# Kernel tuning notes

Hardware: AMD Instinct MI355X
Metric: run time of the kernel (lower is better)

Reference implementation:

```python
import jax, jax.numpy as jnp
import numpy as np

D_MODEL = 1024
N_HEADS = 16
D_K = D_MODEL // N_HEADS
THETA = 10000.0
BATCH, SEQ = 4, 2048


def apply_rope(x, pos, theta=THETA):
    # x: [B, H, S, d_k]; pos: [S] int. Rotate interleaved pairs (x_{2i}, x_{2i+1}).
    half = x.shape[-1] // 2
    inv_freq = theta ** (-jnp.arange(half, dtype=x.dtype) * 2.0 / x.shape[-1])  # [half]
    ang = pos.astype(x.dtype)[:, None] * inv_freq[None, :]                      # [S, half]
    cos, sin = jnp.cos(ang), jnp.sin(ang)
    x1, x2 = x[..., 0::2], x[..., 1::2]
    r1 = x1 * cos - x2 * sin
    r2 = x1 * sin + x2 * cos
    return jnp.stack([r1, r2], axis=-1).reshape(x.shape)


def setup_inputs() -> dict:
    key = jax.random.key(0)
    k1, k2, k3 = jax.random.split(key, 3)
    x = jax.random.normal(k1, (BATCH, SEQ, D_MODEL), dtype=jnp.float32)
    W_qkv = jax.random.normal(k2, (3 * D_MODEL, D_MODEL), dtype=jnp.float32) * (D_MODEL ** -0.5)
    b_qkv = jnp.zeros((3 * D_MODEL,), dtype=jnp.float32)
    W_o = jax.random.normal(k3, (D_MODEL, D_MODEL), dtype=jnp.float32) * (D_MODEL ** -0.5)
    b_o = jnp.zeros((D_MODEL,), dtype=jnp.float32)
    token_positions = jnp.arange(SEQ, dtype=jnp.int64 if jax.config.jax_enable_x64 else jnp.int32)
    return {"x": x, "token_positions": token_positions, "W_qkv": W_qkv,
            "b_qkv": b_qkv, "W_o": W_o, "b_o": b_o}


def reference(x, token_positions, W_qkv, b_qkv, W_o, b_o):
    B, S, _ = x.shape
    qkv = x @ W_qkv.T + b_qkv                                   # [B, S, 3*d_model]
    qkv = qkv.reshape(B, S, 3, N_HEADS, D_K)
    qkv = jnp.transpose(qkv, (2, 0, 3, 1, 4))                   # [3, B, H, S, d_k]
    q, k, v = qkv[0], qkv[1], qkv[2]
    q = apply_rope(q, token_positions)
    k = apply_rope(k, token_positions)
    scores = jnp.einsum('bhqd,bhkd->bhqk', q / jnp.sqrt(jnp.asarray(D_K, x.dtype)), k)
    causal = jnp.tril(jnp.ones((S, S), dtype=bool))             # True where attended
    scores = jnp.where(causal, scores, jnp.asarray(-jnp.inf, scores.dtype))
    attn = jax.nn.softmax(scores, axis=-1)
    out = jnp.einsum('bhqk,bhkd->bhqd', attn, v)                # [B, H, S, d_k]
    out = jnp.transpose(out, (0, 2, 1, 3)).reshape(B, S, D_MODEL)
    return out @ W_o.T + b_o
```

## Files before the change

### kernel.cpp

```cpp
#include <hip/hip_runtime.h>
#include <hip/hip_bf16.h>
#include <cstdint>

#define S_LEN 2048
#define NHEAD 16
#define DMODEL 1024

using short8 = __attribute__((ext_vector_type(8))) short;
using f32x4  = __attribute__((ext_vector_type(4))) float;

__device__ __forceinline__ float bf2f(ushort u) {
    return __uint_as_float(((uint32_t)u) << 16);
}
__device__ __forceinline__ ushort f2bf(float f) {
    uint32_t u = __float_as_uint(f);
    u += 0x7FFF + ((u >> 16) & 1);
    return (ushort)(u >> 16);
}
__device__ __forceinline__ uint32_t cvt_pk_bf16(float lo, float hi) {
    uint32_t r;
    asm("v_cvt_pk_bf16_f32 %0, %1, %2" : "=v"(r) : "v"(lo), "v"(hi));
    return r;
}
__device__ __forceinline__ float exp2_(float x) {
    float r; asm("v_exp_f32 %0, %1" : "=v"(r) : "v"(x)); return r;
}

__global__ void k_cast(const float* __restrict__ in, ushort* __restrict__ out, int n4) {
    int i = blockIdx.x * blockDim.x + threadIdx.x;
    if (i < n4) {
        const float4 v = reinterpret_cast<const float4*>(in)[i];
        ushort4 o;
        o.x = f2bf(v.x); o.y = f2bf(v.y); o.z = f2bf(v.z); o.w = f2bf(v.w);
        reinterpret_cast<ushort4*>(out)[i] = o;
    }
}

__device__ __forceinline__ void gl16(const ushort* g, ushort* l) {
    __builtin_amdgcn_global_load_lds(
        (const __attribute__((address_space(1))) void*)g,
        (__attribute__((address_space(3))) void*)l, 16, 0, 0);
}

template<int OUT_BF16>
__global__ __launch_bounds__(256, 2)
void k_gemm_bt(const ushort* __restrict__ A, const ushort* __restrict__ Bm,
               const float* __restrict__ bias, void* __restrict__ Cout,
               int M, int N, int K)
{
    __shared__ ushort As[128 * 32];
    __shared__ ushort Bs[128 * 32];
    const int t = threadIdx.x;
    const int w = t >> 6, l = t & 63;
    const int lr = l & 15, lg = l >> 4;
    const int bm = blockIdx.y * 128, bn = blockIdx.x * 128;
    const int wr = (w >> 1) * 64, wc = (w & 1) * 64;

    f32x4 acc[4][4] = {};

    const ushort* ag = A + (size_t)(bm + (t >> 2)) * K + (t & 3) * 8;
    const ushort* bg = Bm + (size_t)(bn + (t >> 2)) * K + (t & 3) * 8;
    ushort* asd = &As[t * 8];
    ushort* bsd = &Bs[t * 8];
    const size_t rowskip = (size_t)64 * K;

    for (int k0 = 0; k0 < K; k0 += 32) {
        gl16(ag + k0, asd);
        gl16(ag + rowskip + k0, asd + 2048);
        gl16(bg + k0, bsd);
        gl16(bg + rowskip + k0, bsd + 2048);
        __syncthreads();
        short8 af[4], bf[4];
        #pragma unroll
        for (int m = 0; m < 4; ++m)
            af[m] = *reinterpret_cast<const short8*>(&As[(wr + m * 16 + lr) * 32 + lg * 8]);
        #pragma unroll
        for (int n = 0; n < 4; ++n)
            bf[n] = *reinterpret_cast<const short8*>(&Bs[(wc + n * 16 + lr) * 32 + lg * 8]);
        #pragma unroll
        for (int m = 0; m < 4; ++m)
            #pragma unroll
            for (int n = 0; n < 4; ++n)
                acc[m][n] = __builtin_amdgcn_mfma_f32_16x16x32_bf16(af[m], bf[n], acc[m][n], 0, 0, 0);
        __syncthreads();
    }

    const int col0 = bn + wc + lr;
    float bv[4];
    #pragma unroll
    for (int n = 0; n < 4; ++n) bv[n] = bias[col0 + n * 16];
    #pragma unroll
    for (int m = 0; m < 4; ++m) {
        const int row0 = bm + wr + m * 16 + lg * 4;
        #pragma unroll
        for (int r = 0; r < 4; ++r) {
            const size_t ro = (size_t)(row0 + r) * N;
            #pragma unroll
            for (int n = 0; n < 4; ++n) {
                float v = acc[m][n][r] + bv[n];
                if (OUT_BF16) ((ushort*)Cout)[ro + col0 + n * 16] = f2bf(v);
                else          ((float*)Cout)[ro + col0 + n * 16] = v;
            }
        }
    }
}

__global__ __launch_bounds__(256)
void k_rope_scatter(const ushort* __restrict__ qkv, const int* __restrict__ pos,
                    ushort* __restrict__ Qo, ushort* __restrict__ Ko, ushort* __restrict__ Vt)
{
    __shared__ ushort vlds[64][72];
    const int blk = blockIdx.x;
    const int st = blk & 31, bh = blk >> 5;
    const int b = bh >> 4, h = bh & 15;
    const int t = threadIdx.x;
    const int sl = t >> 2, dc = (t & 3) << 4;
    const int s = st * 64 + sl;
    const size_t base = (size_t)(b * S_LEN + s) * 3072 + h * 64 + dc;
    const float p = (float)pos[s];

    float cs[8], sn[8];
    #pragma unroll
    for (int j = 0; j < 8; ++j) {
        const int fi = (dc >> 1) + j;
        const float invf = __expf(-(float)fi * 0.28782313662425572f);
        __sincosf(p * invf, &sn[j], &cs[j]);
    }

    #pragma unroll
    for (int type = 0; type < 2; ++type) {
        union { uint4 u[2]; ushort us[16]; } in_, out_;
        in_.u[0] = *(const uint4*)(qkv + base + type * 1024);
        in_.u[1] = *(const uint4*)(qkv + base + type * 1024 + 8);
        const float scale = (type == 0) ? 0.125f * 1.44269504088896f : 1.0f;
        #pragma unroll
        for (int j = 0; j < 8; ++j) {
            float x1 = bf2f(in_.us[2 * j]), x2 = bf2f(in_.us[2 * j + 1]);
            out_.us[2 * j]     = f2bf((x1 * cs[j] - x2 * sn[j]) * scale);
            out_.us[2 * j + 1] = f2bf((x1 * sn[j] + x2 * cs[j]) * scale);
        }
        ushort* dst = (type == 0 ? Qo : Ko) + ((size_t)(bh * S_LEN + s)) * 64 + dc;
        *(uint4*)dst = out_.u[0];
        *(uint4*)(dst + 8) = out_.u[1];
    }

    {
        uint4 v0 = *(const uint4*)(qkv + base + 2048);
        uint4 v1 = *(const uint4*)(qkv + base + 2048 + 8);
        *(uint4*)&vlds[sl][dc] = v0;
        *(uint4*)&vlds[sl][dc + 8] = v1;
    }
    __syncthreads();
    {
        const int d = t >> 2, sc0 = (t & 3) << 4;
        union { uint4 u[2]; ushort us[16]; } o;
        #pragma unroll
        for (int j = 0; j < 16; ++j) o.us[j] = vlds[sc0 + j][d];
        ushort* dst = Vt + ((size_t)bh * 64 + d) * S_LEN + st * 64 + sc0;
        *(uint4*)dst = o.u[0];
        *(uint4*)(dst + 8) = o.u[1];
    }
}

__global__ __launch_bounds__(256, 3)
void k_attn(const ushort* __restrict__ Q, const ushort* __restrict__ Kk,
            const ushort* __restrict__ Vt, ushort* __restrict__ O)
{
    __shared__ ushort Ks[2][4096];
    __shared__ ushort Vs[2][4096];
    __shared__ ushort P[4][32][80];

    const int blk = blockIdx.x;
    const int qb = 15 - (blk >> 6);
    const int bh = blk & 63;
    const int b = bh >> 4, h = bh & 15;
    const int t = threadIdx.x, w = t >> 6, l = t & 63;
    const int lr = l & 15, lg = l >> 4;

    const ushort* Kb = Kk + (size_t)bh * S_LEN * 64;
    const ushort* Vb = Vt + (size_t)bh * 64 * S_LEN;
    const ushort* Qb = Q + (size_t)bh * S_LEN * 64;

    const int qbase0 = qb * 128 + w * 16;
    const int qbase1 = qbase0 + 64;

    short8 qf[2][2];
    #pragma unroll
    for (int qg = 0; qg < 2; ++qg)
        #pragma unroll
        for (int dh = 0; dh < 2; ++dh)
            qf[qg][dh] = *(const short8*)(Qb + (size_t)(qbase0 + qg * 64 + lr) * 64 + dh * 32 + lg * 8);

    f32x4 acc[2][4] = {};
    float mx[2] = {-INFINITY, -INFINITY}, ls[2] = {0.f, 0.f};

    const int nt = 2 * qb + 2;

    auto stage = [&](int kb2, int buf) {
        ushort* Kd = Ks[buf]; ushort* Vd = Vs[buf];
        #pragma unroll
        for (int j = 0; j < 2; ++j) {
            const int e = (j * 256 + t) * 8;
            const int row = e >> 6;
            const int col = (e & 63) ^ ((row & 7) << 3);
            gl16(Kb + (size_t)(kb2 + row) * 64 + col, Kd + e);
            gl16(Vb + (size_t)row * S_LEN + kb2 + col, Vd + e);
        }
    };

    stage(0, 0);
    __syncthreads();

    for (int kt = 0; kt < nt; ++kt) {
        const int cur = kt & 1;
        const int kb = kt * 64;
        if (kt + 1 < nt) stage(kb + 64, cur ^ 1);

        const ushort* Kl = Ks[cur];
        short8 kf[4][2];
        #pragma unroll
        for (int i = 0; i < 4; ++i) {
            const int krow = i * 16 + lr, sw = (krow & 7) << 3;
            kf[i][0] = *(const short8*)&Kl[krow * 64 + ((lg * 8) ^ sw)];
            kf[i][1] = *(const short8*)&Kl[krow * 64 + ((32 + lg * 8) ^ sw)];
        }

        auto do_group = [&](int qg, int qbaseg, bool domask) {
            f32x4 st[4] = {};
            __builtin_amdgcn_s_setprio(1);
            #pragma unroll
            for (int i = 0; i < 4; ++i) {
                st[i] = __builtin_amdgcn_mfma_f32_16x16x32_bf16(kf[i][0], qf[qg][0], st[i], 0, 0, 0);
                st[i] = __builtin_amdgcn_mfma_f32_16x16x32_bf16(kf[i][1], qf[qg][1], st[i], 0, 0, 0);
            }
            __builtin_amdgcn_s_setprio(0);
            if (domask) {
                const int qrow = qbaseg + lr;
                #pragma unroll
                for (int i = 0; i < 4; ++i)
                    #pragma unroll
                    for (int r = 0; r < 4; ++r)
                        if (kb + i * 16 + lg * 4 + r > qrow) st[i][r] = -INFINITY;
            }
            float a0 = fmaxf(fmaxf(st[0][0], st[0][1]), fmaxf(st[0][2], st[0][3]));
            float a1 = fmaxf(fmaxf(st[1][0], st[1][1]), fmaxf(st[1][2], st[1][3]));
            float a2 = fmaxf(fmaxf(st[2][0], st[2][1]), fmaxf(st[2][2], st[2][3]));
            float a3 = fmaxf(fmaxf(st[3][0], st[3][1]), fmaxf(st[3][2], st[3][3]));
            float tm = fmaxf(fmaxf(a0, a1), fmaxf(a2, a3));
            tm = fmaxf(tm, __shfl_xor(tm, 16));
            tm = fmaxf(tm, __shfl_xor(tm, 32));
            float mn = mx[qg];
            if (!__all(tm <= mn + 12.0f)) {
                mn = fmaxf(mx[qg], tm);
                const float sc = exp2_(mx[qg] - mn);
                ls[qg] *= sc;
                #pragma unroll
                for (int d = 0; d < 4; ++d)
                    #pragma unroll
                    for (int r = 0; r < 4; ++r) acc[qg][d][r] *= sc;
                mx[qg] = mn;
            }
            float ps = 0.f;
            #pragma unroll
            for (int i = 0; i < 4; ++i) {
                const float e0 = exp2_(st[i][0] - mn);
                const float e1 = exp2_(st[i][1] - mn);
                const float e2 = exp2_(st[i][2] - mn);
                const float e3 = exp2_(st[i][3] - mn);
                ps += (e0 + e1) + (e2 + e3);
                uint2 pk;
                pk.x = cvt_pk_bf16(e0, e1);
                pk.y = cvt_pk_bf16(e2, e3);
                *(uint2*)&P[w][qg * 16 + lr][i * 16 + lg * 4] = pk;
            }
            ps += __shfl_xor(ps, 16);
            ps += __shfl_xor(ps, 32);
            ls[qg] += ps;
        };

        const bool g0 = (kt < nt - 1);
        do_group(1, qbase1, kt == nt - 1);
        if (g0) do_group(0, qbase0, kt == nt - 2);

        short8 pf1[2], pf0[2];
        pf1[0] = *(const short8*)&P[w][16 + lr][lg * 8];
        pf1[1] = *(const short8*)&P[w][16 + lr][32 + lg * 8];
        if (g0) {
            pf0[0] = *(const short8*)&P[w][lr][lg * 8];
            pf0[1] = *(const short8*)&P[w][lr][32 + lg * 8];
        }
        const ushort* Vl = Vs[cur];
        __builtin_amdgcn_s_setprio(1);
        #pragma unroll
        for (int d = 0; d < 4; ++d) {
            const int vrow = d * 16 + lr, sw = (vrow & 7) << 3;
            short8 v0 = *(const short8*)&Vl[vrow * 64 + ((lg * 8) ^ sw)];
            short8 v1 = *(const short8*)&Vl[vrow * 64 + ((32 + lg * 8) ^ sw)];
            acc[1][d] = __builtin_amdgcn_mfma_f32_16x16x32_bf16(v0, pf1[0], acc[1][d], 0, 0, 0);
            acc[1][d] = __builtin_amdgcn_mfma_f32_16x16x32_bf16(v1, pf1[1], acc[1][d], 0, 0, 0);
            if (g0) {
                acc[0][d] = __builtin_amdgcn_mfma_f32_16x16x32_bf16(v0, pf0[0], acc[0][d], 0, 0, 0);
                acc[0][d] = __builtin_amdgcn_mfma_f32_16x16x32_bf16(v1, pf0[1], acc[0][d], 0, 0, 0);
            }
        }
        __builtin_amdgcn_s_setprio(0);
        __syncthreads();
    }

    #pragma unroll
    for (int qg = 0; qg < 2; ++qg) {
        const float inv = 1.f / ls[qg];
        const int q = qbase0 + qg * 64 + lr;
        #pragma unroll
        for (int d = 0; d < 4; ++d) {
            ushort4 ov;
            #pragma unroll
            for (int r = 0; r < 4; ++r) ((ushort*)&ov)[r] = f2bf(acc[qg][d][r] * inv);
            *(ushort4*)&O[((size_t)(b * S_LEN) + q) * 1024 + h * 64 + d * 16 + lg * 4] = ov;
        }
    }
}

extern "C" void kernel_launch(void* const* d_in, const int* in_sizes, int n_in,
                              void* d_out, int out_size, void* d_ws, size_t ws_size,
                              hipStream_t stream)
{
    const float* x    = (const float*)d_in[0];
    const int*   pos  = (const int*)d_in[1];
    const float* Wqkv = (const float*)d_in[2];
    const float* bqkv = (const float*)d_in[3];
    const float* Wo   = (const float*)d_in[4];
    const float* bo   = (const float*)d_in[5];
    float* out = (float*)d_out;

    char* ws = (char*)d_ws;
    ushort* xb   = (ushort*)(ws);
    ushort* wqb  = (ushort*)(ws + 16777216);
    ushort* wob  = (ushort*)(ws + 23068672);
    ushort* qkvb = (ushort*)(ws + 25165824);
    ushort* Qb   = (ushort*)(ws + 75497472);
    ushort* Kb   = (ushort*)(ws + 92274688);
    ushort* Vtb  = (ushort*)(ws + 109051904);
    ushort* AOb  = (ushort*)(ws + 125829120);

    k_cast<<<8192, 256, 0, stream>>>(x, xb, 2097152);
    k_cast<<<3072, 256, 0, stream>>>(Wqkv, wqb, 786432);
    k_cast<<<1024, 256, 0, stream>>>(Wo, wob, 262144);
    k_gemm_bt<1><<<dim3(24, 64), 256, 0, stream>>>(xb, wqb, bqkv, qkvb, 8192, 3072, 1024);
    k_rope_scatter<<<2048, 256, 0, stream>>>(qkvb, pos, Qb, Kb, Vtb);
    k_attn<<<1024, 256, 0, stream>>>(Qb, Kb, Vtb, AOb);
    k_gemm_bt<0><<<dim3(8, 64), 256, 0, stream>>>(AOb, wob, bo, out, 8192, 1024, 1024);
}
```

Measured before the change: 194.6 us.

## Add 256x256 double-buffered swizzled GEMM kernel for QKV projection

Replaces the 128x128 QKV projection GEMM with a new 512-thread kernel using 256x256 tiles, a K-step of 64, and double-buffered LDS filled via global_load_lds. It adds XOR swizzling against LDS bank conflicts, fine-grained vmcnt waits interleaved with MFMA phases, and an XCD-aware block remap. The goal is more data reuse per tile and overlap of the next tile's loads with compute. In exchange it uses 128KB of LDS per block and many accumulator registers, which limits occupancy. The output-projection GEMM is simplified to an fp32-only version.

```diff
diff --git a/kernel.cpp b/kernel.cpp
--- a/kernel.cpp
+++ b/kernel.cpp
@@ -24,6 +24,9 @@
 }
 __device__ __forceinline__ float exp2_(float x) {
     float r; asm("v_exp_f32 %0, %1" : "=v"(r) : "v"(x)); return r;
+}
+template<int N> __device__ __forceinline__ void vwait() {
+    asm volatile("s_waitcnt vmcnt(%0)" :: "n"(N) : "memory");
 }
 
 __global__ void k_cast(const float* __restrict__ in, ushort* __restrict__ out, int n4) {
@@ -42,10 +45,119 @@
         (__attribute__((address_space(3))) void*)l, 16, 0, 0);
 }
 
-template<int OUT_BF16>
+__global__ __launch_bounds__(512, 2)
+void k_gemm256(const ushort* __restrict__ A, const ushort* __restrict__ Bm,
+               const float* __restrict__ bias, ushort* __restrict__ C,
+               int M, int N, int K, int nbn)
+{
+    __shared__ ushort As[2][16384];
+    __shared__ ushort Bs[2][16384];
+
+    const int bid = blockIdx.x;
+    const int cpx = gridDim.x >> 3;
+    const int wg = (bid & 7) * cpx + (bid >> 3);
+    const int bn = (wg % nbn) * 256, bm = (wg / nbn) * 256;
+    const int t = threadIdx.x, w = t >> 6, l = t & 63;
+    const int wr = w >> 2, wc = w & 3;
+    const int lr = l & 15, lg = l >> 4;
+
+    f32x4 acc[8][4] = {};
+
+    auto stage2 = [&](int kt, int b, int p) {
+        #pragma unroll
+        for (int uu = 0; uu < 2; ++uu) {
+            const int u = 2 * p + uu;
+            const int e = (u & 3) * 4096 + t * 8;
+            const int r = e >> 6;
+            const int c = (e & 63) ^ ((r & 7) << 3);
+            if (u < 4) gl16(Bm + (size_t)(bn + r) * K + kt * 64 + c, &Bs[b][e]);
+            else       gl16(A  + (size_t)(bm + r) * K + kt * 64 + c, &As[b][e]);
+        }
+    };
+
+    #pragma unroll
+    for (int p = 0; p < 4; ++p) stage2(0, 0, p);
+    vwait<0>();
+    __builtin_amdgcn_s_barrier();
+
+    const int NT = K >> 6;
+    short8 bfr[4][2];
+
+    for (int tt = 0; tt < NT; ++tt) {
+        const int b = tt & 1;
+        const ushort* Al = As[b];
+        const ushort* Bl = Bs[b];
+        const bool st = (tt < NT - 1);
+
+        #pragma unroll
+        for (int p = 0; p < 4; ++p) {
+            if (st) {
+                stage2(tt + 1, b ^ 1, p);
+                if      (p == 0) vwait<5>();
+                else if (p == 1) vwait<6>();
+                else if (p == 2) vwait<7>();
+                else             vwait<8>();
+            } else {
+                if      (p == 0) vwait<3>();
+                else if (p == 1) vwait<2>();
+                else if (p == 2) vwait<1>();
+                else             vwait<0>();
+            }
+            __builtin_amdgcn_s_barrier();
+            __builtin_amdgcn_sched_barrier(0);
+
+            if (p == 0) {
+                #pragma unroll
+                for (int n = 0; n < 4; ++n) {
+                    const int rB = wc * 64 + n * 16 + lr;
+                    #pragma unroll
+                    for (int kk = 0; kk < 2; ++kk)
+                        bfr[n][kk] = *(const short8*)&Bl[rB * 64 + ((kk * 32 + lg * 8) ^ ((rB & 7) << 3))];
+                }
+            }
+            short8 afr[2][2];
+            #pragma unroll
+            for (int jj = 0; jj < 2; ++jj) {
+                const int rA = wr * 16 + 32 * (2 * p + jj) + lr;
+                #pragma unroll
+                for (int kk = 0; kk < 2; ++kk)
+                    afr[jj][kk] = *(const short8*)&Al[rA * 64 + ((kk * 32 + lg * 8) ^ ((rA & 7) << 3))];
+            }
+            __builtin_amdgcn_s_setprio(1);
+            #pragma unroll
+            for (int jj = 0; jj < 2; ++jj)
+                #pragma unroll
+                for (int n = 0; n < 4; ++n)
+                    #pragma unroll
+                    for (int kk = 0; kk < 2; ++kk)
+                        acc[2 * p + jj][n] = __builtin_amdgcn_mfma_f32_16x16x32_bf16(
+                            afr[jj][kk], bfr[n][kk], acc[2 * p + jj][n], 0, 0, 0);
+            __builtin_amdgcn_s_setprio(0);
+            __builtin_amdgcn_sched_barrier(0);
+            __builtin_amdgcn_s_barrier();
+        }
+    }
+
+    const int col0 = bn + wc * 64 + lr;
+    float bv[4];
+    #pragma unroll
+    for (int n = 0; n < 4; ++n) bv[n] = bias[col0 + n * 16];
+    #pragma unroll
+    for (int j = 0; j < 8; ++j) {
+        const int row0 = bm + wr * 16 + 32 * j + lg * 4;
+        #pragma unroll
+        for (int r = 0; r < 4; ++r) {
+            const size_t ro = (size_t)(row0 + r) * N;
+            #pragma unroll
+            for (int n = 0; n < 4; ++n)
+                C[ro + col0 + n * 16] = f2bf(acc[j][n][r] + bv[n]);
+        }
+    }
+}
+
 __global__ __launch_bounds__(256, 2)
 void k_gemm_bt(const ushort* __restrict__ A, const ushort* __restrict__ Bm,
-               const float* __restrict__ bias, void* __restrict__ Cout,
+               const float* __restrict__ bias, float* __restrict__ Cout,
                int M, int N, int K)
 {
     __shared__ ushort As[128 * 32];
@@ -96,11 +208,8 @@
         for (int r = 0; r < 4; ++r) {
             const size_t ro = (size_t)(row0 + r) * N;
             #pragma unroll
-            for (int n = 0; n < 4; ++n) {
-                float v = acc[m][n][r] + bv[n];
-                if (OUT_BF16) ((ushort*)Cout)[ro + col0 + n * 16] = f2bf(v);
-                else          ((float*)Cout)[ro + col0 + n * 16] = v;
-            }
+            for (int n = 0; n < 4; ++n)
+                Cout[ro + col0 + n * 16] = acc[m][n][r] + bv[n];
         }
     }
 }
@@ -346,8 +455,8 @@
     k_cast<<<8192, 256, 0, stream>>>(x, xb, 2097152);
     k_cast<<<3072, 256, 0, stream>>>(Wqkv, wqb, 786432);
     k_cast<<<1024, 256, 0, stream>>>(Wo, wob, 262144);
-    k_gemm_bt<1><<<dim3(24, 64), 256, 0, stream>>>(xb, wqb, bqkv, qkvb, 8192, 3072, 1024);
+    k_gemm256<<<384, 512, 0, stream>>>(xb, wqb, bqkv, qkvb, 8192, 3072, 1024, 12);
     k_rope_scatter<<<2048, 256, 0, stream>>>(qkvb, pos, Qb, Kb, Vtb);
     k_attn<<<1024, 256, 0, stream>>>(Qb, Kb, Vtb, AOb);
-    k_gemm_bt<0><<<dim3(8, 64), 256, 0, stream>>>(AOb, wob, bo, out, 8192, 1024, 1024);
-}
+    k_gemm_bt<<<dim3(8, 64), 256, 0, stream>>>(AOb, wob, bo, out, 8192, 1024, 1024);
+}
```

Result: slower. 202.7 us (+4.1%).
